# Kernel tuning notes

Hardware: AMD Instinct MI355X
Metric: run time of the kernel (lower is better)

## Reference

```python
import jax, jax.numpy as jnp
import numpy as np

N_NODES = 50000
N_EDGES = 600000
D_IN = 128
D_OUT = 128
P_DROP = 0.1
BN_EPS = 1e-5


def setup_inputs() -> dict:
    key = jax.random.key(0)
    ks = jax.random.split(key, 6)
    x = jax.random.normal(ks[0], (N_NODES, D_IN), dtype=jnp.float32)
    weight = jax.random.normal(ks[1], (D_IN, D_OUT), dtype=jnp.float32) * (1.0 / np.sqrt(D_IN))
    bias = jnp.zeros((D_OUT,), dtype=jnp.float32)
    gamma = jnp.ones((D_OUT,), dtype=jnp.float32)
    beta = jnp.zeros((D_OUT,), dtype=jnp.float32)
    dropout_u = jax.random.uniform(ks[2], (N_NODES, D_OUT), dtype=jnp.float32)
    edge_index = jax.random.randint(ks[3], (2, N_EDGES), 0, N_NODES, dtype=jnp.int64)
    return {"x": x, "weight": weight, "bias": bias, "gamma": gamma,
            "beta": beta, "dropout_u": dropout_u, "edge_index": edge_index}


def reference(x, weight, bias, gamma, beta, dropout_u, edge_index):
    N = x.shape[0]
    # --- GCNConv (add_self_loops=True, symmetric normalization) ---
    loop = jnp.arange(N, dtype=edge_index.dtype)
    src = jnp.concatenate([edge_index[0], loop])  # [E+N]
    dst = jnp.concatenate([edge_index[1], loop])  # [E+N]
    xw = x @ weight                               # [N, D_OUT] small GEMM
    deg = jnp.zeros((N,), dtype=xw.dtype).at[dst].add(1.0)
    dinv = jnp.where(deg > 0, jax.lax.rsqrt(jnp.maximum(deg, 1.0)), 0.0)
    norm = dinv[src] * dinv[dst]                  # [E+N]
    msgs = xw[src] * norm[:, None]                # gather: [E+N, D_OUT]
    z = jax.ops.segment_sum(msgs, dst, num_segments=N) + bias
    # --- activation -> BatchNorm (training stats) -> dropout ---
    z = jax.nn.relu(z)
    mean = jnp.mean(z, axis=0)
    var = jnp.mean((z - mean) ** 2, axis=0)       # biased var, as BN uses
    z = (z - mean) * jax.lax.rsqrt(var + BN_EPS) * gamma + beta
    keep = (dropout_u > P_DROP).astype(z.dtype)
    z = z * keep * (1.0 / (1.0 - P_DROP))
    return z.astype(x.dtype)
```

## Files before the change

kernel.cpp:

```cpp
#include <hip/hip_runtime.h>
#include <cstdint>
#include <cstddef>

#define D 128
#define P_DROP 0.1f
#define INV_KEEP (1.0f / 0.9f)
#define BN_EPS 1e-5f

typedef __attribute__((ext_vector_type(8))) short bf16x8;
typedef __attribute__((ext_vector_type(4))) float f32x4;

__device__ __forceinline__ unsigned f2bf(float f) {
    unsigned u = __float_as_uint(f);
    return (u + 0x7fffu + ((u >> 16) & 1u)) >> 16;
}
__device__ __forceinline__ float bf_lo(unsigned v) { return __uint_as_float(v << 16); }
__device__ __forceinline__ float bf_hi(unsigned v) { return __uint_as_float(v & 0xffff0000u); }

__global__ void k_init(int* __restrict__ hist, float* __restrict__ bnacc, int N) {
    int i = blockIdx.x * blockDim.x + threadIdx.x;
    if (i < N) hist[i] = 0;
    if (i < 256) bnacc[i] = 0.f;
}

__global__ void k_hist(const int* __restrict__ dst, int* __restrict__ hist, int E) {
    int i = blockIdx.x * blockDim.x + threadIdx.x;
    if (i < E) atomicAdd(&hist[dst[i]], 1);
}

__global__ void k_scanA(const int* __restrict__ hist, int* __restrict__ tmp,
                        int* __restrict__ blocksum, int N) {
    __shared__ int sd[256];
    int tid = threadIdx.x;
    int i = blockIdx.x * 256 + tid;
    sd[tid] = (i < N) ? hist[i] : 0;
    __syncthreads();
    for (int o = 1; o < 256; o <<= 1) {
        int t = (tid >= o) ? sd[tid - o] : 0;
        __syncthreads();
        sd[tid] += t;
        __syncthreads();
    }
    tmp[i] = sd[tid];
    if (tid == 255) blocksum[blockIdx.x] = sd[255];
}

__global__ void k_scanB(const int* __restrict__ blocksum, int* __restrict__ blockoff,
                        int NBLK) {
    __shared__ int sd[256];
    int tid = threadIdx.x;
    int v = (tid < NBLK) ? blocksum[tid] : 0;
    sd[tid] = v;
    __syncthreads();
    for (int o = 1; o < 256; o <<= 1) {
        int t = (tid >= o) ? sd[tid - o] : 0;
        __syncthreads();
        sd[tid] += t;
        __syncthreads();
    }
    if (tid < NBLK) blockoff[tid] = sd[tid] - v;
}

__global__ void k_scanC(const int* __restrict__ tmp, const int* __restrict__ blockoff,
                        const int* __restrict__ hist,
                        int* __restrict__ off, int* __restrict__ cursor, int N) {
    int i = blockIdx.x * 256 + threadIdx.x;
    if (i < N) {
        int incl = tmp[i] + blockoff[blockIdx.x];
        off[i + 1] = incl;
        cursor[i] = incl - hist[i];
    }
    if (i == 0) off[0] = 0;
}

__global__ void k_place(const int* __restrict__ src, const int* __restrict__ dst,
                        int* __restrict__ cursor, int* __restrict__ ebuf, int E) {
    int i = blockIdx.x * blockDim.x + threadIdx.x;
    if (i < E) {
        int p = atomicAdd(&cursor[dst[i]], 1);
        ebuf[p] = src[i];
    }
}

__global__ __launch_bounds__(256) void k_gemm(
    const float* __restrict__ x, const float* __restrict__ w,
    const int* __restrict__ hist, unsigned short* __restrict__ xwb,
    float* __restrict__ dinv, int N) {
    __shared__ unsigned short xs[64][136];
    __shared__ unsigned short wt[128][136];
    int tid = threadIdx.x;
    int row0 = blockIdx.x * 64;

#pragma unroll
    for (int i = 0; i < 32; ++i) {
        int flat = tid + i * 256;
        int n = flat & 127;
        int kp = flat >> 7;
        float a0 = w[(size_t)(2 * kp) * D + n];
        float a1 = w[(size_t)(2 * kp + 1) * D + n];
        *(unsigned*)&wt[n][2 * kp] = f2bf(a0) | (f2bf(a1) << 16);
    }
#pragma unroll
    for (int i = 0; i < 8; ++i) {
        int flat = tid + i * 256;
        int r = flat >> 5;
        int kq = flat & 31;
        int row = row0 + r;
        float4 v = (row < N) ? *(const float4*)&x[(size_t)row * D + kq * 4]
                             : make_float4(0.f, 0.f, 0.f, 0.f);
        uint2 pk;
        pk.x = f2bf(v.x) | (f2bf(v.y) << 16);
        pk.y = f2bf(v.z) | (f2bf(v.w) << 16);
        *(uint2*)&xs[r][kq * 4] = pk;
    }
    __syncthreads();

    int wv = tid >> 6, lane = tid & 63;
    int l15 = lane & 15, quad = lane >> 4;
    int mrow = wv * 16 + l15;
    f32x4 acc[8];
#pragma unroll
    for (int t = 0; t < 8; ++t) acc[t] = (f32x4){0.f, 0.f, 0.f, 0.f};
#pragma unroll
    for (int k0 = 0; k0 < D; k0 += 32) {
        bf16x8 af = *(bf16x8*)&xs[mrow][k0 + quad * 8];
#pragma unroll
        for (int nt = 0; nt < 8; ++nt) {
            bf16x8 bfr = *(bf16x8*)&wt[nt * 16 + l15][k0 + quad * 8];
            acc[nt] = __builtin_amdgcn_mfma_f32_16x16x32_bf16(af, bfr, acc[nt], 0, 0, 0);
        }
    }
#pragma unroll
    for (int reg = 0; reg < 4; ++reg) {
        int node = row0 + wv * 16 + quad * 4 + reg;
        if (node < N) {
            float dv = rsqrtf((float)(hist[node] + 1));
            if (l15 == 0) dinv[node] = dv;
#pragma unroll
            for (int nt = 0; nt < 8; ++nt) {
                float val = acc[nt][reg] * dv;
                xwb[(size_t)node * D + nt * 16 + l15] = (unsigned short)f2bf(val);
            }
        }
    }
}

__global__ __launch_bounds__(256) void k_aggregate(
    const unsigned short* __restrict__ xwb, const float* __restrict__ dinv,
    const int* __restrict__ off, const int* __restrict__ ebuf,
    const float* __restrict__ bias, float* __restrict__ y,
    float* __restrict__ bnacc, int N, int nwaves) {
    int tid = threadIdx.x;
    int lane = tid & 63;
    int wv = tid >> 6;
    int gw = blockIdx.x * 4 + wv;
    int chunk = (N + nwaves - 1) / nwaves;
    int a = gw * chunk;
    int b = min(a + chunk, N);
    float2 b2 = ((const float2*)bias)[lane];
    float ps0 = 0.f, ps1 = 0.f, pq0 = 0.f, pq1 = 0.f;

    if (a < b) {
        int run = b - a;
        int v_off = off[a + min(lane, run)];
        int v_dv  = ((const int*)dinv)[a + min(lane, run - 1)];
        for (int n = a; n < b; ++n) {
            int nl = n - a;
            int s0 = __builtin_amdgcn_readlane(v_off, nl);
            int s1 = __builtin_amdgcn_readlane(v_off, nl + 1);
            unsigned selfv = *(const unsigned*)(xwb + (size_t)n * D + lane * 2);
            float ax = bf_lo(selfv), ay = bf_hi(selfv);
            for (int c = s0; c < s1; c += 64) {
                int m = min(64, s1 - c);
                int vidx = ebuf[c + lane];
                int e = 0;
                for (; e + 16 <= m; e += 16) {
                    unsigned vv[16];
#pragma unroll
                    for (int j = 0; j < 16; ++j) {
                        int idx = __builtin_amdgcn_readlane(vidx, e + j);
                        vv[j] = *(const unsigned*)(xwb + (size_t)idx * D + lane * 2);
                    }
#pragma unroll
                    for (int j = 0; j < 16; ++j) { ax += bf_lo(vv[j]); ay += bf_hi(vv[j]); }
                }
                for (; e + 4 <= m; e += 4) {
                    unsigned vv[4];
#pragma unroll
                    for (int j = 0; j < 4; ++j) {
                        int idx = __builtin_amdgcn_readlane(vidx, e + j);
                        vv[j] = *(const unsigned*)(xwb + (size_t)idx * D + lane * 2);
                    }
#pragma unroll
                    for (int j = 0; j < 4; ++j) { ax += bf_lo(vv[j]); ay += bf_hi(vv[j]); }
                }
                for (; e < m; ++e) {
                    int idx = __builtin_amdgcn_readlane(vidx, e);
                    unsigned v = *(const unsigned*)(xwb + (size_t)idx * D + lane * 2);
                    ax += bf_lo(v); ay += bf_hi(v);
                }
            }
            float dv = __int_as_float(__builtin_amdgcn_readlane(v_dv, nl));
            float y0 = fmaxf(fmaf(ax, dv, b2.x), 0.f);
            float y1 = fmaxf(fmaf(ay, dv, b2.y), 0.f);
            *(float2*)(y + (size_t)n * D + lane * 2) = make_float2(y0, y1);
            ps0 += y0; ps1 += y1;
            pq0 += y0 * y0; pq1 += y1 * y1;
        }
    }

    __shared__ float red[4][256];
    red[wv][lane * 2] = ps0;       red[wv][lane * 2 + 1] = ps1;
    red[wv][128 + lane * 2] = pq0; red[wv][128 + lane * 2 + 1] = pq1;
    __syncthreads();
    {
        float s = red[0][tid] + red[1][tid] + red[2][tid] + red[3][tid];
        atomicAdd(&bnacc[tid], s);
    }
}

__global__ void k_bnfinal(const float* __restrict__ bnacc, const float* __restrict__ gamma,
                          const float* __restrict__ beta, float* __restrict__ scsh, int N) {
    int c = threadIdx.x;
    if (c < 128) {
        float invN = 1.0f / (float)N;
        float mean = bnacc[c] * invN;
        float var = bnacc[128 + c] * invN - mean * mean;
        var = fmaxf(var, 0.f);
        float sc = gamma[c] * rsqrtf(var + BN_EPS);
        scsh[c] = sc;
        scsh[128 + c] = beta[c] - mean * sc;
    }
}

__global__ __launch_bounds__(256) void k_finalize(
    float* __restrict__ out, const float* __restrict__ u,
    const float* __restrict__ scsh, int total4) {
    int i = blockIdx.x * 256 + threadIdx.x;
    if (i >= total4) return;
    float4 v = ((const float4*)out)[i];
    float4 uu = ((const float4*)u)[i];
    int c = (i & 31) * 4;
    float s0 = scsh[c], s1 = scsh[c + 1], s2 = scsh[c + 2], s3 = scsh[c + 3];
    float h0 = scsh[128 + c], h1 = scsh[128 + c + 1];
    float h2 = scsh[128 + c + 2], h3 = scsh[128 + c + 3];
    v.x = fmaf(v.x, s0, h0) * (uu.x > P_DROP ? INV_KEEP : 0.f);
    v.y = fmaf(v.y, s1, h1) * (uu.y > P_DROP ? INV_KEEP : 0.f);
    v.z = fmaf(v.z, s2, h2) * (uu.z > P_DROP ? INV_KEEP : 0.f);
    v.w = fmaf(v.w, s3, h3) * (uu.w > P_DROP ? INV_KEEP : 0.f);
    ((float4*)out)[i] = v;
}

extern "C" void kernel_launch(void* const* d_in, const int* in_sizes, int n_in,
                              void* d_out, int out_size, void* d_ws, size_t ws_size,
                              hipStream_t stream) {
    const float* x      = (const float*)d_in[0];
    const float* weight = (const float*)d_in[1];
    const float* bias   = (const float*)d_in[2];
    const float* gamma  = (const float*)d_in[3];
    const float* beta   = (const float*)d_in[4];
    const float* du     = (const float*)d_in[5];
    const int*   eidx   = (const int*)d_in[6];
    float* out = (float*)d_out;

    const int N = in_sizes[0] / D;
    const int E = in_sizes[6] / 2;
    const int* esrc = eidx;
    const int* edst = eidx + E;

    char* p = (char*)d_ws;
    auto alloc = [&](size_t bytes) {
        char* q = p;
        p += (bytes + 255) & ~(size_t)255;
        return q;
    };
    unsigned short* xwb = (unsigned short*)alloc((size_t)N * D * sizeof(unsigned short));
    int*   hist     = (int*)alloc((size_t)N * sizeof(int));
    int*   cursor   = (int*)alloc((size_t)N * sizeof(int));
    int*   off      = (int*)alloc((size_t)(N + 1) * sizeof(int));
    const int NBLK = (N + 255) / 256;
    int*   tmp      = (int*)alloc((size_t)NBLK * 256 * sizeof(int));
    int*   blocksum = (int*)alloc((size_t)NBLK * sizeof(int));
    int*   blockoff = (int*)alloc((size_t)NBLK * sizeof(int));
    int*   ebuf     = (int*)alloc((size_t)(E + 64) * sizeof(int));
    float* dinv     = (float*)alloc((size_t)N * sizeof(float));
    float* bnacc    = (float*)alloc(256 * sizeof(float));
    float* scsh     = (float*)alloc(256 * sizeof(float));

    const int EB = (E + 255) / 256;
    hipLaunchKernelGGL(k_init, dim3(NBLK), dim3(256), 0, stream, hist, bnacc, N);
    hipLaunchKernelGGL(k_hist, dim3(EB), dim3(256), 0, stream, edst, hist, E);
    hipLaunchKernelGGL(k_scanA, dim3(NBLK), dim3(256), 0, stream, hist, tmp, blocksum, N);
    hipLaunchKernelGGL(k_scanB, dim3(1), dim3(256), 0, stream, blocksum, blockoff, NBLK);
    hipLaunchKernelGGL(k_scanC, dim3(NBLK), dim3(256), 0, stream, tmp, blockoff, hist, off, cursor, N);
    hipLaunchKernelGGL(k_place, dim3(EB), dim3(256), 0, stream, esrc, edst, cursor, ebuf, E);
    hipLaunchKernelGGL(k_gemm, dim3((N + 63) / 64), dim3(256), 0, stream,
                       x, weight, hist, xwb, dinv, N);
    const int AGG_BLOCKS = 2048;
    hipLaunchKernelGGL(k_aggregate, dim3(AGG_BLOCKS), dim3(256), 0, stream,
                       xwb, dinv, off, ebuf, bias, out, bnacc, N, AGG_BLOCKS * 4);
    hipLaunchKernelGGL(k_bnfinal, dim3(1), dim3(128), 0, stream, bnacc, gamma, beta, scsh, N);
    const int total4 = N * (D / 4);
    hipLaunchKernelGGL(k_finalize, dim3((total4 + 255) / 256), dim3(256), 0, stream,
                       out, du, scsh, total4);
}
```

Measured before the change: 257.8 us.

## Switch aggregation to edge-balanced segmented reduction with boundary atomics

Replaces the node-chunked CSR aggregation with an edge-parallel scheme. Each wave takes exactly 64 dst-sorted edges, does a segmented sum, and writes node partials, using atomics only for segments that cross wave boundaries. Self-loop, bias, ReLU and BN statistics move to a separate post-aggregation pass, and the output buffer is zeroed in init. This removes load imbalance from skewed degrees. In exchange it adds a full extra read/write pass over y, a memset of the output, extra sorted-dst storage, and float atomics that make the sums nondeterministic.

```diff
diff --git a/kernel.cpp b/kernel.cpp
--- a/kernel.cpp
+++ b/kernel.cpp
@@ -17,10 +17,17 @@
 __device__ __forceinline__ float bf_lo(unsigned v) { return __uint_as_float(v << 16); }
 __device__ __forceinline__ float bf_hi(unsigned v) { return __uint_as_float(v & 0xffff0000u); }
 
-__global__ void k_init(int* __restrict__ hist, float* __restrict__ bnacc, int N) {
-    int i = blockIdx.x * blockDim.x + threadIdx.x;
-    if (i < N) hist[i] = 0;
-    if (i < 256) bnacc[i] = 0.f;
+__global__ void k_init(float4* __restrict__ y4, int n4,
+                       int* __restrict__ hist, int N,
+                       float* __restrict__ bnacc,
+                       int* __restrict__ ssrc, int* __restrict__ sdst, int E) {
+    int stride = gridDim.x * blockDim.x;
+    int i0 = blockIdx.x * blockDim.x + threadIdx.x;
+    float4 z = make_float4(0.f, 0.f, 0.f, 0.f);
+    for (int i = i0; i < n4; i += stride) y4[i] = z;
+    for (int i = i0; i < N; i += stride) hist[i] = 0;
+    if (i0 < 256) bnacc[i0] = 0.f;
+    if (i0 < 64) { ssrc[E + i0] = 0; sdst[E + i0] = -1; }
 }
 
 __global__ void k_hist(const int* __restrict__ dst, int* __restrict__ hist, int E) {
@@ -62,23 +69,20 @@
 }
 
 __global__ void k_scanC(const int* __restrict__ tmp, const int* __restrict__ blockoff,
-                        const int* __restrict__ hist,
-                        int* __restrict__ off, int* __restrict__ cursor, int N) {
+                        const int* __restrict__ hist, int* __restrict__ cursor, int N) {
     int i = blockIdx.x * 256 + threadIdx.x;
-    if (i < N) {
-        int incl = tmp[i] + blockoff[blockIdx.x];
-        off[i + 1] = incl;
-        cursor[i] = incl - hist[i];
-    }
-    if (i == 0) off[0] = 0;
+    if (i < N) cursor[i] = tmp[i] + blockoff[blockIdx.x] - hist[i];
 }
 
 __global__ void k_place(const int* __restrict__ src, const int* __restrict__ dst,
-                        int* __restrict__ cursor, int* __restrict__ ebuf, int E) {
+                        int* __restrict__ cursor,
+                        int* __restrict__ ssrc, int* __restrict__ sdst, int E) {
     int i = blockIdx.x * blockDim.x + threadIdx.x;
     if (i < E) {
-        int p = atomicAdd(&cursor[dst[i]], 1);
-        ebuf[p] = src[i];
+        int d = dst[i];
+        int p = atomicAdd(&cursor[d], 1);
+        ssrc[p] = src[i];
+        sdst[p] = d;
     }
 }
 
@@ -147,75 +151,100 @@
 
 __global__ __launch_bounds__(256) void k_aggregate(
     const unsigned short* __restrict__ xwb, const float* __restrict__ dinv,
-    const int* __restrict__ off, const int* __restrict__ ebuf,
-    const float* __restrict__ bias, float* __restrict__ y,
-    float* __restrict__ bnacc, int N, int nwaves) {
+    const int* __restrict__ ssrc, const int* __restrict__ sdst,
+    float* __restrict__ y, int E) {
+    int lane = threadIdx.x & 63;
+    int wv = threadIdx.x >> 6;
+    int w = blockIdx.x * 4 + wv;
+    int e0 = w * 64;
+    if (e0 >= E) return;
+
+    int vsrc = ssrc[e0 + lane];
+    int vdst = sdst[e0 + lane];
+    int prevd = (w > 0) ? __builtin_amdgcn_readfirstlane(sdst[e0 - 1]) : -5;
+    int nextd = __builtin_amdgcn_readfirstlane(sdst[e0 + 64]);
+    int cidx = vdst < 0 ? 0 : vdst;
+    float dvv = dinv[cidx];
+
+    float a0 = 0.f, a1 = 0.f;
+    int cur = __builtin_amdgcn_readlane(vdst, 0);
+    bool excl = (prevd != cur);
+
+    unsigned vrow[32];
+#pragma unroll
+    for (int half = 0; half < 2; ++half) {
+        int base = half * 32;
+#pragma unroll
+        for (int j = 0; j < 32; ++j) {
+            int idx = __builtin_amdgcn_readlane(vsrc, base + j);
+            vrow[j] = *(const unsigned*)(xwb + (size_t)idx * D + lane * 2);
+        }
+#pragma unroll
+        for (int j = 0; j < 32; ++j) {
+            int gj = base + j;
+            int dj = __builtin_amdgcn_readlane(vdst, gj);
+            if (dj != cur) {
+                float dv = __int_as_float(
+                    __builtin_amdgcn_readlane(__float_as_int(dvv), gj - 1));
+                float s0 = a0 * dv, s1 = a1 * dv;
+                float* yp = y + (size_t)cur * D + lane * 2;
+                if (excl) { *(float2*)yp = make_float2(s0, s1); }
+                else { atomicAdd(yp, s0); atomicAdd(yp + 1, s1); }
+                a0 = 0.f; a1 = 0.f; cur = dj; excl = true;
+            }
+            unsigned v = vrow[j];
+            a0 += bf_lo(v); a1 += bf_hi(v);
+        }
+    }
+    if (cur >= 0) {
+        float dv = __int_as_float(__builtin_amdgcn_readlane(__float_as_int(dvv), 63));
+        float s0 = a0 * dv, s1 = a1 * dv;
+        float* yp = y + (size_t)cur * D + lane * 2;
+        if (excl && (nextd != cur)) { *(float2*)yp = make_float2(s0, s1); }
+        else { atomicAdd(yp, s0); atomicAdd(yp + 1, s1); }
+    }
+}
+
+__global__ __launch_bounds__(256) void k_postagg(
+    float* __restrict__ y, const unsigned short* __restrict__ xwb,
+    const float* __restrict__ dinv, const float* __restrict__ bias,
+    float* __restrict__ bnacc, int total4) {
     int tid = threadIdx.x;
-    int lane = tid & 63;
-    int wv = tid >> 6;
-    int gw = blockIdx.x * 4 + wv;
-    int chunk = (N + nwaves - 1) / nwaves;
-    int a = gw * chunk;
-    int b = min(a + chunk, N);
-    float2 b2 = ((const float2*)bias)[lane];
-    float ps0 = 0.f, ps1 = 0.f, pq0 = 0.f, pq1 = 0.f;
-
-    if (a < b) {
-        int run = b - a;
-        int v_off = off[a + min(lane, run)];
-        int v_dv  = ((const int*)dinv)[a + min(lane, run - 1)];
-        for (int n = a; n < b; ++n) {
-            int nl = n - a;
-            int s0 = __builtin_amdgcn_readlane(v_off, nl);
-            int s1 = __builtin_amdgcn_readlane(v_off, nl + 1);
-            unsigned selfv = *(const unsigned*)(xwb + (size_t)n * D + lane * 2);
-            float ax = bf_lo(selfv), ay = bf_hi(selfv);
-            for (int c = s0; c < s1; c += 64) {
-                int m = min(64, s1 - c);
-                int vidx = ebuf[c + lane];
-                int e = 0;
-                for (; e + 16 <= m; e += 16) {
-                    unsigned vv[16];
-#pragma unroll
-                    for (int j = 0; j < 16; ++j) {
-                        int idx = __builtin_amdgcn_readlane(vidx, e + j);
-                        vv[j] = *(const unsigned*)(xwb + (size_t)idx * D + lane * 2);
-                    }
-#pragma unroll
-                    for (int j = 0; j < 16; ++j) { ax += bf_lo(vv[j]); ay += bf_hi(vv[j]); }
-                }
-                for (; e + 4 <= m; e += 4) {
-                    unsigned vv[4];
-#pragma unroll
-                    for (int j = 0; j < 4; ++j) {
-                        int idx = __builtin_amdgcn_readlane(vidx, e + j);
-                        vv[j] = *(const unsigned*)(xwb + (size_t)idx * D + lane * 2);
-                    }
-#pragma unroll
-                    for (int j = 0; j < 4; ++j) { ax += bf_lo(vv[j]); ay += bf_hi(vv[j]); }
-                }
-                for (; e < m; ++e) {
-                    int idx = __builtin_amdgcn_readlane(vidx, e);
-                    unsigned v = *(const unsigned*)(xwb + (size_t)idx * D + lane * 2);
-                    ax += bf_lo(v); ay += bf_hi(v);
-                }
-            }
-            float dv = __int_as_float(__builtin_amdgcn_readlane(v_dv, nl));
-            float y0 = fmaxf(fmaf(ax, dv, b2.x), 0.f);
-            float y1 = fmaxf(fmaf(ay, dv, b2.y), 0.f);
-            *(float2*)(y + (size_t)n * D + lane * 2) = make_float2(y0, y1);
-            ps0 += y0; ps1 += y1;
-            pq0 += y0 * y0; pq1 += y1 * y1;
-        }
-    }
-
-    __shared__ float red[4][256];
-    red[wv][lane * 2] = ps0;       red[wv][lane * 2 + 1] = ps1;
-    red[wv][128 + lane * 2] = pq0; red[wv][128 + lane * 2 + 1] = pq1;
+    int stride = gridDim.x * 256;
+    int c4 = tid & 31;
+    float4 b4 = ((const float4*)bias)[c4];
+    float s0 = 0.f, s1 = 0.f, s2 = 0.f, s3 = 0.f;
+    float q0 = 0.f, q1 = 0.f, q2 = 0.f, q3 = 0.f;
+    for (int i = blockIdx.x * 256 + tid; i < total4; i += stride) {
+        int node = i >> 5;
+        float4 z = ((float4*)y)[i];
+        uint2 sv = *(const uint2*)(xwb + (size_t)node * D + c4 * 4);
+        float dv = dinv[node];
+        z.x = fmaxf(fmaf(bf_lo(sv.x), dv, z.x) + b4.x, 0.f);
+        z.y = fmaxf(fmaf(bf_hi(sv.x), dv, z.y) + b4.y, 0.f);
+        z.z = fmaxf(fmaf(bf_lo(sv.y), dv, z.z) + b4.z, 0.f);
+        z.w = fmaxf(fmaf(bf_hi(sv.y), dv, z.w) + b4.w, 0.f);
+        ((float4*)y)[i] = z;
+        s0 += z.x; s1 += z.y; s2 += z.z; s3 += z.w;
+        q0 += z.x * z.x; q1 += z.y * z.y; q2 += z.z * z.z; q3 += z.w * z.w;
+    }
+    __shared__ float red[256][8];
+    red[tid][0] = s0; red[tid][1] = s1; red[tid][2] = s2; red[tid][3] = s3;
+    red[tid][4] = q0; red[tid][5] = q1; red[tid][6] = q2; red[tid][7] = q3;
     __syncthreads();
-    {
-        float s = red[0][tid] + red[1][tid] + red[2][tid] + red[3][tid];
-        atomicAdd(&bnacc[tid], s);
+    if (tid < 128) {
+        int r0 = tid >> 2, sl = tid & 3;
+        float acc = 0.f;
+#pragma unroll
+        for (int m = 0; m < 8; ++m) acc += red[r0 + 32 * m][sl];
+        atomicAdd(&bnacc[tid], acc);
+    } else {
+        int t = tid - 128;
+        int r0 = t >> 2, sl = 4 + (t & 3);
+        float acc = 0.f;
+#pragma unroll
+        for (int m = 0; m < 8; ++m) acc += red[r0 + 32 * m][sl];
+        atomicAdd(&bnacc[128 + t], acc);
     }
 }
 
@@ -277,30 +306,33 @@
     unsigned short* xwb = (unsigned short*)alloc((size_t)N * D * sizeof(unsigned short));
     int*   hist     = (int*)alloc((size_t)N * sizeof(int));
     int*   cursor   = (int*)alloc((size_t)N * sizeof(int));
-    int*   off      = (int*)alloc((size_t)(N + 1) * sizeof(int));
     const int NBLK = (N + 255) / 256;
     int*   tmp      = (int*)alloc((size_t)NBLK * 256 * sizeof(int));
     int*   blocksum = (int*)alloc((size_t)NBLK * sizeof(int));
     int*   blockoff = (int*)alloc((size_t)NBLK * sizeof(int));
-    int*   ebuf     = (int*)alloc((size_t)(E + 64) * sizeof(int));
+    int*   ssrc     = (int*)alloc((size_t)(E + 64) * sizeof(int));
+    int*   sdst     = (int*)alloc((size_t)(E + 64) * sizeof(int));
     float* dinv     = (float*)alloc((size_t)N * sizeof(float));
     float* bnacc    = (float*)alloc(256 * sizeof(float));
     float* scsh     = (float*)alloc(256 * sizeof(float));
 
     const int EB = (E + 255) / 256;
-    hipLaunchKernelGGL(k_init, dim3(NBLK), dim3(256), 0, stream, hist, bnacc, N);
+    const int total4 = N * (D / 4);
+    hipLaunchKernelGGL(k_init, dim3(1024), dim3(256), 0, stream,
+                       (float4*)out, total4, hist, N, bnacc, ssrc, sdst, E);
     hipLaunchKernelGGL(k_hist, dim3(EB), dim3(256), 0, stream, edst, hist, E);
     hipLaunchKernelGGL(k_scanA, dim3(NBLK), dim3(256), 0, stream, hist, tmp, blocksum, N);
     hipLaunchKernelGGL(k_scanB, dim3(1), dim3(256), 0, stream, blocksum, blockoff, NBLK);
-    hipLaunchKernelGGL(k_scanC, dim3(NBLK), dim3(256), 0, stream, tmp, blockoff, hist, off, cursor, N);
-    hipLaunchKernelGGL(k_place, dim3(EB), dim3(256), 0, stream, esrc, edst, cursor, ebuf, E);
+    hipLaunchKernelGGL(k_scanC, dim3(NBLK), dim3(256), 0, stream, tmp, blockoff, hist, cursor, N);
+    hipLaunchKernelGGL(k_place, dim3(EB), dim3(256), 0, stream, esrc, edst, cursor, ssrc, sdst, E);
     hipLaunchKernelGGL(k_gemm, dim3((N + 63) / 64), dim3(256), 0, stream,
                        x, weight, hist, xwb, dinv, N);
-    const int AGG_BLOCKS = 2048;
-    hipLaunchKernelGGL(k_aggregate, dim3(AGG_BLOCKS), dim3(256), 0, stream,
-                       xwb, dinv, off, ebuf, bias, out, bnacc, N, AGG_BLOCKS * 4);
+    const int NWAVE = (E + 63) / 64;
+    hipLaunchKernelGGL(k_aggregate, dim3((NWAVE + 3) / 4), dim3(256), 0, stream,
+                       xwb, dinv, ssrc, sdst, out, E);
+    hipLaunchKernelGGL(k_postagg, dim3(1024), dim3(256), 0, stream,
+                       out, xwb, dinv, bias, bnacc, total4);
     hipLaunchKernelGGL(k_bnfinal, dim3(1), dim3(128), 0, stream, bnacc, gamma, beta, scsh, N);
-    const int total4 = N * (D / 4);
     hipLaunchKernelGGL(k_finalize, dim3((total4 + 255) / 256), dim3(256), 0, stream,
                        out, du, scsh, total4);
 }
```

Result: no change. 257.4 us (-0.1%).
